# Kernel optimization log

Measured on AMD Instinct MI355X. Metric: run time of the kernel, lower is better.

## Reference

```python
import jax, jax.numpy as jnp
import numpy as np

EMBED_DIM = 768
NUM_HEAD = 12
HEAD_DIM = EMBED_DIM // NUM_HEAD


def setup_inputs() -> dict:
    key = jax.random.key(0)
    ks = jax.random.split(key, 9)
    B, S, E = 1, 4096, EMBED_DIM
    s = 1.0 / np.sqrt(E)
    inp = {
        "x": jax.random.normal(ks[0], (B, S, E), dtype=jnp.float32),
        "mask": jnp.zeros((B, S), dtype=jnp.bool_),  # True = masked out (padding)
        "Wq": jax.random.normal(ks[1], (E, E), dtype=jnp.float32) * s,
        "bq": jnp.zeros((E,), dtype=jnp.float32),
        "Wk": jax.random.normal(ks[2], (E, E), dtype=jnp.float32) * s,
        "bk": jnp.zeros((E,), dtype=jnp.float32),
        "Wv": jax.random.normal(ks[3], (E, E), dtype=jnp.float32) * s,
        "bv": jnp.zeros((E,), dtype=jnp.float32),
        "Wo": jax.random.normal(ks[4], (E, E), dtype=jnp.float32) * s,
        "bo": jnp.zeros((E,), dtype=jnp.float32),
    }
    return inp


def reference(x, mask, Wq, bq, Wk, bk, Wv, bv, Wo, bo):
    B, S, E = x.shape
    H, D = NUM_HEAD, HEAD_DIM
    # QKV projections -> [B, H, S, D]
    q = (x @ Wq.T + bq).reshape(B, S, H, D).transpose(0, 2, 1, 3)
    k = (x @ Wk.T + bk).reshape(B, S, H, D).transpose(0, 2, 1, 3)
    v = (x @ Wv.T + bv).reshape(B, S, H, D).transpose(0, 2, 1, 3)
    # NOTE: original scales by sqrt(embed_dim), not sqrt(head_dim)
    attn = jnp.einsum("bhqd,bhkd->bhqk", q, k) / jnp.sqrt(jnp.float32(E))
    # mask: [B, S] -> broadcast over (head, query) dims; True -> -inf
    attn = jnp.where(mask[:, None, None, :], -jnp.inf, attn)
    attn = jax.nn.softmax(attn, axis=-1)  # same math as manual max-subtract softmax
    out = jnp.einsum("bhqk,bhkd->bhqd", attn, v)  # [B, H, S, D]
    out = out.transpose(0, 2, 1, 3).reshape(B, S, E)
    return out @ Wo.T + bo
```

## Files before the change

### kernel.cpp

```cpp
#include <hip/hip_runtime.h>
#include <hip/hip_bf16.h>
#include <math.h>

typedef __bf16 bf16;
typedef __attribute__((ext_vector_type(8))) __bf16 bf16x8;
typedef __attribute__((ext_vector_type(4))) __bf16 bf16x4;
typedef __attribute__((ext_vector_type(4))) float f32x4;
typedef __attribute__((ext_vector_type(16))) float f32x16;

typedef __attribute__((address_space(1))) void* as1ptr;
typedef __attribute__((address_space(3))) void* as3ptr;

__device__ __forceinline__ void gload16(const void* g, void* lds) {
  __builtin_amdgcn_global_load_lds((as1ptr)(unsigned long long)(g),
                                   (as3ptr)(unsigned long long)(lds), 16, 0, 0);
}

#define MFMA16(a, b, c) __builtin_amdgcn_mfma_f32_16x16x32_bf16((a), (b), (c), 0, 0, 0)
#define MFMA32(a, b, c) __builtin_amdgcn_mfma_f32_32x32x16_bf16((a), (b), (c), 0, 0, 0)
#define EXP2(x) __builtin_amdgcn_exp2f(x)
#define WAITV4 asm volatile("s_waitcnt vmcnt(4)" ::: "memory")
#define WAITV2 asm volatile("s_waitcnt vmcnt(2)" ::: "memory")
#define WAITV0 asm volatile("s_waitcnt vmcnt(0)" ::: "memory")
#define BAR() __builtin_amdgcn_s_barrier()
#define PRIO1() __builtin_amdgcn_s_setprio(1)
#define PRIO0() __builtin_amdgcn_s_setprio(0)

#define SEQ 4096
#define EMB 768
#define QSC (0.036084391824351615f * 1.4426950408889634f)

#define NCVT 2688
__global__ __launch_bounds__(256)
void cvt_all_kernel(const float* __restrict__ x, const float* __restrict__ Wq,
                    const float* __restrict__ Wk, const float* __restrict__ Wv,
                    const float* __restrict__ Wo,
                    bf16* __restrict__ xb, bf16* __restrict__ Wqb, bf16* __restrict__ Wkb,
                    bf16* __restrict__ Wvb, bf16* __restrict__ Wob,
                    const unsigned char* __restrict__ mask,
                    unsigned long long* __restrict__ tf64) {
  int b = blockIdx.x;
  if (b == NCVT) {
    int t = threadIdx.x;
    if (t < 64) {
      unsigned v = 0;
      const unsigned char* mp = mask + t * 64;
      for (int i = 0; i < 64; i++) v |= mp[i];
      unsigned long long bits = __ballot(v != 0);
      if (t == 0) *tf64 = bits;
    }
    return;
  }
  const float* in;
  bf16* out;
  int base;
  if (b < 1536) {
    in = x; out = xb; base = b;
  } else {
    int r = b - 1536, seg = r / 288, off = r % 288;
    in  = (seg == 0) ? Wq  : (seg == 1) ? Wk  : (seg == 2) ? Wv  : Wo;
    out = (seg == 0) ? Wqb : (seg == 1) ? Wkb : (seg == 2) ? Wvb : Wob;
    base = off;
  }
  int i = (base * 256 + threadIdx.x) * 8;
  float4 a = *(const float4*)(in + i);
  float4 c = *(const float4*)(in + i + 4);
  bf16x8 v;
  v[0] = (bf16)a.x; v[1] = (bf16)a.y; v[2] = (bf16)a.z; v[3] = (bf16)a.w;
  v[4] = (bf16)c.x; v[5] = (bf16)c.y; v[6] = (bf16)c.z; v[7] = (bf16)c.w;
  *(bf16x8*)(out + i) = v;
}

template <int MODE>
__global__ __launch_bounds__(256)
void gemm_bt_kernel(const bf16* __restrict__ A,
                    const bf16* __restrict__ B0, const bf16* __restrict__ B1,
                    const bf16* __restrict__ B2,
                    const float* __restrict__ bias0, const float* __restrict__ bias1,
                    const float* __restrict__ bias2,
                    float* __restrict__ outF, bf16* __restrict__ Qh,
                    char* __restrict__ Kswz, char* __restrict__ Vswz) {
  __shared__ __attribute__((aligned(16))) char Asb[3][8192];
  __shared__ __attribute__((aligned(16))) char Bsb[3][8192];
  const int tid = threadIdx.x;
  const int wid = tid >> 6, lane = tid & 63;
  const int g = lane >> 4, c16 = lane & 15;
  const int wr = wid >> 1, wc = wid & 1;
  const int bm0 = blockIdx.x * 128;

  const bf16* Bp;
  const float* bias;
  int nb, mat = 0;
  if (MODE == 1) {
    mat = blockIdx.y / 6;
    nb = (blockIdx.y % 6) * 128;
    Bp = (mat == 0) ? B0 : (mat == 1 ? B1 : B2);
    bias = (mat == 0) ? bias0 : (mat == 1 ? bias1 : bias2);
  } else {
    nb = blockIdx.y * 128;
    Bp = B0;
    bias = bias0;
  }

  const int arow = tid >> 2, acol = (tid & 3) * 16;

#define STAGE_G(k, b)                                                              \
  do {                                                                             \
    gload16((const char*)A + (size_t)(bm0 + arow) * (EMB * 2) + (k)*64 + acol,     \
            &Asb[b][wid * 1024]);                                                  \
    gload16((const char*)A + (size_t)(bm0 + 64 + arow) * (EMB * 2) + (k)*64 + acol,\
            &Asb[b][4096 + wid * 1024]);                                           \
    gload16((const char*)Bp + (size_t)(nb + arow) * (EMB * 2) + (k)*64 + acol,     \
            &Bsb[b][wid * 1024]);                                                  \
    gload16((const char*)Bp + (size_t)(nb + 64 + arow) * (EMB * 2) + (k)*64 + acol,\
            &Bsb[b][4096 + wid * 1024]);                                           \
  } while (0)

  f32x4 acc[4][4];
#pragma unroll
  for (int i = 0; i < 4; i++)
#pragma unroll
    for (int j = 0; j < 4; j++) acc[i][j] = f32x4{0.f, 0.f, 0.f, 0.f};

#define COMPUTE_G(cur)                                                         \
  do {                                                                         \
    bf16x8 a[4], b[4];                                                         \
    _Pragma("unroll") for (int i = 0; i < 4; i++)                              \
        a[i] = *(const bf16x8*)(&Asb[cur][(wr * 64 + i * 16 + c16) * 64 + g * 16]); \
    _Pragma("unroll") for (int j = 0; j < 4; j++)                              \
        b[j] = *(const bf16x8*)(&Bsb[cur][(wc * 64 + j * 16 + c16) * 64 + g * 16]); \
    PRIO1();                                                                   \
    _Pragma("unroll") for (int i = 0; i < 4; i++)                              \
        _Pragma("unroll") for (int j = 0; j < 4; j++)                          \
            acc[i][j] = MFMA16(a[i], b[j], acc[i][j]);                         \
    PRIO0();                                                                   \
  } while (0)

  STAGE_G(0, 0);
  STAGE_G(1, 1);
  int cur = 0;
  for (int kk = 0; kk < EMB / 32 - 1; ++kk) {
    WAITV4;
    BAR();
    if (kk < EMB / 32 - 2) {
      int stb = (cur == 0) ? 2 : cur - 1;
      STAGE_G(kk + 2, stb);
    }
    COMPUTE_G(cur);
    cur = (cur == 2) ? 0 : cur + 1;
  }
  WAITV0;
  BAR();
  COMPUTE_G(cur);
#undef STAGE_G
#undef COMPUTE_G

#pragma unroll
  for (int i = 0; i < 4; i++) {
#pragma unroll
    for (int j = 0; j < 4; j++) {
      int colL = nb + wc * 64 + j * 16 + c16;
      float bval = bias[colL];
#pragma unroll
      for (int r = 0; r < 4; r++) {
        int row = bm0 + wr * 64 + i * 16 + 4 * g + r;
        float val = acc[i][j][r] + bval;
        if (MODE == 0) {
          outF[(size_t)row * EMB + colL] = val;
        } else {
          int hh = colL >> 6, d = colL & 63;
          if (mat == 0) {
            Qh[((size_t)hh * SEQ + row) * 64 + d] = (bf16)(val * QSC);
          } else if (mat == 1) {
            *(bf16*)(Kswz + ((size_t)hh * SEQ + row) * 128 +
                     ((d * 2) ^ ((row & 7) << 4))) = (bf16)val;
          } else {
            int kk2 = row & 63;
            int cc = (kk2 & 48) | (kk2 & 3) | ((kk2 & 4) << 1) | ((kk2 & 8) >> 1);
            *(bf16*)(Vswz + ((size_t)hh * 64 + d) * 8192 + (size_t)(row >> 6) * 128 +
                     ((cc * 2) ^ ((d & 7) << 4))) = (bf16)val;
          }
        }
      }
    }
  }
}

__global__ __launch_bounds__(512)
void attn_kernel(const char* __restrict__ Kswz, const char* __restrict__ Vswz,
                 const bf16* __restrict__ Qh, const unsigned char* __restrict__ mask,
                 const unsigned long long* __restrict__ tf64,
                 bf16* __restrict__ P0, bf16* __restrict__ P1, float* __restrict__ lm) {
  __shared__ __attribute__((aligned(16))) char LBUF[49152];
  char* LK = LBUF;
  char* LV = LBUF + 24576;
  const int tid = threadIdx.x;
  const int wid = tid >> 6, lane = tid & 63;
  const int qh = wid >> 1, kh = wid & 1;
  const int l31 = lane & 31, hi = lane >> 5;
  const int bsw = ((blockIdx.x & 7) * 96) + (blockIdx.x >> 3);
  const int h = bsw >> 6;
  const int rem = bsw & 63;
  const int qb = rem >> 1;
  const int ks = rem & 1;
  const unsigned long long tfb = *tf64;
  const int NT = 32;

  bf16x8 qa[4];
  {
    const bf16* qp = Qh + ((size_t)h * SEQ + qb * 128 + qh * 32 + l31) * 64 + hi * 8;
    qa[0] = *(const bf16x8*)(qp);
    qa[1] = *(const bf16x8*)(qp + 16);
    qa[2] = *(const bf16x8*)(qp + 32);
    qa[3] = *(const bf16x8*)(qp + 48);
  }

  f32x16 ot0, ot1;
#pragma unroll
  for (int r = 0; r < 16; r++) { ot0[r] = 0.f; ot1[r] = 0.f; }
  float l_ = 0.f;

  const char* ksrc = Kswz + (size_t)h * SEQ * 128 + (size_t)ks * 2048 * 128 + tid * 16;
  const char* vsrc = Vswz + ((size_t)h * 64 + (tid >> 3)) * 8192 + ks * 4096 + (tid & 7) * 16;

#define STAGE(t, b)                                              \
  do {                                                           \
    gload16(ksrc + (size_t)(t)*8192, LK + (b)*8192 + wid * 1024);\
    gload16(vsrc + (size_t)(t)*128,  LV + (b)*8192 + wid * 1024);\
  } while (0)

  const int krow = kh * 32 + l31;
  const int ksw = (krow & 7) << 4;
  const int vsw = (l31 & 7) << 4;
  const int vcb = kh * 64 + hi * 16;

#define COMPUTE(t, cur)                                                          \
  do {                                                                           \
    const char* Kb = LK + (cur)*8192;                                            \
    const char* Vb = LV + (cur)*8192;                                            \
    bf16x8 kf0 = *(const bf16x8*)(Kb + krow * 128 + ((hi * 16) ^ ksw));          \
    bf16x8 kf1 = *(const bf16x8*)(Kb + krow * 128 + ((32 + hi * 16) ^ ksw));     \
    bf16x8 kf2 = *(const bf16x8*)(Kb + krow * 128 + ((64 + hi * 16) ^ ksw));     \
    bf16x8 kf3 = *(const bf16x8*)(Kb + krow * 128 + ((96 + hi * 16) ^ ksw));     \
    f32x16 s;                                                                    \
    _Pragma("unroll") for (int r = 0; r < 16; r++) s[r] = 0.f;                   \
    PRIO1();                                                                     \
    s = MFMA32(kf0, qa[0], s);                                                   \
    s = MFMA32(kf1, qa[1], s);                                                   \
    s = MFMA32(kf2, qa[2], s);                                                   \
    s = MFMA32(kf3, qa[3], s);                                                   \
    PRIO0();                                                                     \
    if (tfb & (1ull << (ks * 32 + (t)))) {                                       \
      _Pragma("unroll") for (int r = 0; r < 16; r++) {                           \
        int key = ks * 2048 + (t)*64 + kh * 32 + (r & 3) + 8 * (r >> 2) + 4 * hi;\
        if (mask[key]) s[r] = -INFINITY;                                         \
      }                                                                          \
    }                                                                            \
    float p[16];                                                                 \
    _Pragma("unroll") for (int r = 0; r < 16; r++) p[r] = EXP2(s[r]);            \
    float ls = (((p[0] + p[1]) + (p[2] + p[3])) + ((p[4] + p[5]) + (p[6] + p[7]))) + \
               (((p[8] + p[9]) + (p[10] + p[11])) + ((p[12] + p[13]) + (p[14] + p[15]))); \
    l_ += ls;                                                                    \
    bf16x8 pb0, pb1;                                                             \
    _Pragma("unroll") for (int e = 0; e < 8; ++e) {                              \
      pb0[e] = (bf16)p[e];                                                       \
      pb1[e] = (bf16)p[8 + e];                                                   \
    }                                                                            \
    bf16x8 vf00 = *(const bf16x8*)(Vb + l31 * 128 + ((vcb) ^ vsw));              \
    bf16x8 vf01 = *(const bf16x8*)(Vb + l31 * 128 + ((vcb + 32) ^ vsw));         \
    bf16x8 vf10 = *(const bf16x8*)(Vb + (32 + l31) * 128 + ((vcb) ^ vsw));       \
    bf16x8 vf11 = *(const bf16x8*)(Vb + (32 + l31) * 128 + ((vcb + 32) ^ vsw));  \
    PRIO1();                                                                     \
    ot0 = MFMA32(vf00, pb0, ot0);                                                \
    ot0 = MFMA32(vf01, pb1, ot0);                                                \
    ot1 = MFMA32(vf10, pb0, ot1);                                                \
    ot1 = MFMA32(vf11, pb1, ot1);                                                \
    PRIO0();                                                                     \
  } while (0)

  STAGE(0, 0);
  STAGE(1, 1);
  int cur = 0;
  for (int t = 0; t < NT - 1; ++t) {
    WAITV2;
    BAR();
    if (t < NT - 2) {
      int stb = (cur == 0) ? 2 : cur - 1;
      STAGE(t + 2, stb);
    }
    COMPUTE(t, cur);
    cur = (cur == 2) ? 0 : cur + 1;
  }
  WAITV0;
  BAR();
  COMPUTE(NT - 1, cur);
#undef STAGE
#undef COMPUTE

  l_ += __shfl_xor(l_, 32);

  __syncthreads();
  float* ml = (float*)(LBUF + 32768);
  ml[wid * 64 + lane] = l_;
  __syncthreads();
  const int pw = wid ^ 1;
  float lt = l_ + ml[pw * 64 + lane];
  char* obase = LBUF + qh * 8192 + lane * 128;
  const int osw = (lane & 7) << 4;
  if (kh == 1) {
#pragma unroll
    for (int u = 0; u < 4; ++u) {
      *(f32x4*)(obase + ((u * 16) ^ osw)) =
          f32x4{ot0[4 * u], ot0[4 * u + 1], ot0[4 * u + 2], ot0[4 * u + 3]};
      *(f32x4*)(obase + (((4 + u) * 16) ^ osw)) =
          f32x4{ot1[4 * u], ot1[4 * u + 1], ot1[4 * u + 2], ot1[4 * u + 3]};
    }
  }
  __syncthreads();
  if (kh == 0) {
    float inv = 1.f / lt;
    int tok = qb * 128 + qh * 32 + l31;
    bf16* Op = ks ? P1 : P0;
    bf16* op = Op + (size_t)tok * EMB + h * 64;
#pragma unroll
    for (int u = 0; u < 4; ++u) {
      f32x4 w0 = *(const f32x4*)(obase + ((u * 16) ^ osw));
      f32x4 w1 = *(const f32x4*)(obase + (((4 + u) * 16) ^ osw));
      bf16x4 o0, o1;
#pragma unroll
      for (int e = 0; e < 4; ++e) {
        o0[e] = (bf16)((ot0[4 * u + e] + w0[e]) * inv);
        o1[e] = (bf16)((ot1[4 * u + e] + w1[e]) * inv);
      }
      *(bf16x4*)(op + 8 * u + 4 * hi) = o0;
      *(bf16x4*)(op + 32 + 8 * u + 4 * hi) = o1;
    }
    if (lane < 32) {
      lm[(((size_t)ks * 12 + h) * 4096 + tok) * 2 + 1] = lt;
    }
  }
}

__global__ __launch_bounds__(256)
void merge_kernel(bf16* __restrict__ P0, const bf16* __restrict__ P1,
                  const float* __restrict__ lm) {
  int idx = (blockIdx.x * 256 + threadIdx.x) * 8;
  int tok = idx / EMB;
  int e0 = idx % EMB;
  int h = e0 >> 6;
  float l0 = lm[((size_t)h * 4096 + tok) * 2 + 1];
  float l1 = lm[(((size_t)12 + h) * 4096 + tok) * 2 + 1];
  float inv = 1.f / (l0 + l1);
  float w0 = l0 * inv;
  float w1 = l1 * inv;
  bf16x8 a = *(const bf16x8*)(P0 + idx);
  bf16x8 b = *(const bf16x8*)(P1 + idx);
  bf16x8 o;
#pragma unroll
  for (int e = 0; e < 8; ++e) o[e] = (bf16)(w0 * (float)a[e] + w1 * (float)b[e]);
  *(bf16x8*)(P0 + idx) = o;
}

extern "C" void kernel_launch(void* const* d_in, const int* in_sizes, int n_in,
                              void* d_out, int out_size, void* d_ws, size_t ws_size,
                              hipStream_t stream) {
  (void)in_sizes; (void)n_in; (void)out_size; (void)ws_size;
  const float* x = (const float*)d_in[0];
  const unsigned char* mask = (const unsigned char*)d_in[1];
  const float* Wq = (const float*)d_in[2];
  const float* bq = (const float*)d_in[3];
  const float* Wk = (const float*)d_in[4];
  const float* bk = (const float*)d_in[5];
  const float* Wv = (const float*)d_in[6];
  const float* bv = (const float*)d_in[7];
  const float* Wo = (const float*)d_in[8];
  const float* bo = (const float*)d_in[9];
  float* out = (float*)d_out;
  char* ws = (char*)d_ws;

  bf16* xb   = (bf16*)(ws + 0);
  bf16* Wqb  = (bf16*)(ws + 6291456);
  bf16* Wkb  = (bf16*)(ws + 7471104);
  bf16* Wvb  = (bf16*)(ws + 8650752);
  bf16* Wob  = (bf16*)(ws + 9830400);
  bf16* Qh   = (bf16*)(ws + 11010048);
  char* Kswz = ws + 17301504;
  char* Vswz = ws + 23592960;
  bf16* Obuf = (bf16*)(ws + 29884416);
  unsigned long long* tf64 = (unsigned long long*)(ws + 36175872);
  float* lmArr = (float*)(ws + 36179968);
  bf16* P1 = xb;

  cvt_all_kernel<<<NCVT + 1, 256, 0, stream>>>(x, Wq, Wk, Wv, Wo, xb, Wqb, Wkb, Wvb,
                                               Wob, mask, tf64);
  gemm_bt_kernel<1><<<dim3(32, 18), 256, 0, stream>>>(
      xb, Wqb, Wkb, Wvb, bq, bk, bv, nullptr, Qh, Kswz, Vswz);
  attn_kernel<<<768, 512, 0, stream>>>(Kswz, Vswz, Qh, mask, tf64, Obuf, P1, lmArr);
  merge_kernel<<<1536, 256, 0, stream>>>(Obuf, P1, lmArr);
  gemm_bt_kernel<0><<<dim3(32, 6), 256, 0, stream>>>(
      Obuf, Wob, nullptr, nullptr, bo, nullptr, nullptr, out, nullptr, nullptr, nullptr);
}
```

Measured before the change: 124.2 us.

## Split attention keys four ways with 4-wave blocks each computing two query tiles

The attention kernel moves from 512-thread blocks with a 2-way key split to 256-thread blocks with a 4-way key split. Each wave now computes two 32-row query tiles against the same K/V fragments, so every LDS load feeds twice as many MFMAs. The staging pipeline drops from three buffers to two, with a full vmcnt wait each iteration. The merge kernel now combines four partials, two of them parked in the output buffer, which adds merge traffic and reduces how far loads run ahead of compute.

```diff
diff --git a/kernel.cpp b/kernel.cpp
--- a/kernel.cpp
+++ b/kernel.cpp
@@ -20,7 +20,6 @@
 #define MFMA32(a, b, c) __builtin_amdgcn_mfma_f32_32x32x16_bf16((a), (b), (c), 0, 0, 0)
 #define EXP2(x) __builtin_amdgcn_exp2f(x)
 #define WAITV4 asm volatile("s_waitcnt vmcnt(4)" ::: "memory")
-#define WAITV2 asm volatile("s_waitcnt vmcnt(2)" ::: "memory")
 #define WAITV0 asm volatile("s_waitcnt vmcnt(0)" ::: "memory")
 #define BAR() __builtin_amdgcn_s_barrier()
 #define PRIO1() __builtin_amdgcn_s_setprio(1)
@@ -186,48 +185,52 @@
   }
 }
 
-__global__ __launch_bounds__(512)
+__global__ __launch_bounds__(256)
 void attn_kernel(const char* __restrict__ Kswz, const char* __restrict__ Vswz,
                  const bf16* __restrict__ Qh, const unsigned char* __restrict__ mask,
                  const unsigned long long* __restrict__ tf64,
-                 bf16* __restrict__ P0, bf16* __restrict__ P1, float* __restrict__ lm) {
-  __shared__ __attribute__((aligned(16))) char LBUF[49152];
-  char* LK = LBUF;
-  char* LV = LBUF + 24576;
+                 bf16* __restrict__ P0, bf16* __restrict__ P1,
+                 bf16* __restrict__ P2, bf16* __restrict__ P3, float* __restrict__ lm) {
+  __shared__ __attribute__((aligned(16))) char LBUF[32768];
   const int tid = threadIdx.x;
   const int wid = tid >> 6, lane = tid & 63;
   const int qh = wid >> 1, kh = wid & 1;
   const int l31 = lane & 31, hi = lane >> 5;
-  const int bsw = ((blockIdx.x & 7) * 96) + (blockIdx.x >> 3);
-  const int h = bsw >> 6;
-  const int rem = bsw & 63;
-  const int qb = rem >> 1;
-  const int ks = rem & 1;
+  const int bsw = ((blockIdx.x & 7) * 192) + (blockIdx.x >> 3);
+  const int h = bsw >> 7;
+  const int rem = bsw & 127;
+  const int qb = rem >> 2;
+  const int ks = rem & 3;
   const unsigned long long tfb = *tf64;
-  const int NT = 32;
-
-  bf16x8 qa[4];
+  const int NT = 16;
+
+  const char* ksrc = Kswz + (size_t)h * SEQ * 128 + (size_t)ks * 1024 * 128 + tid * 16;
+  const char* vsrc = Vswz + ((size_t)h * 64 + (tid >> 3)) * 8192 + ks * 2048 + (tid & 7) * 16;
+
+#define STAGE(t, b)                                                             \
+  do {                                                                          \
+    gload16(ksrc + (size_t)(t)*8192,        LBUF + (b)*16384 + wid * 1024);     \
+    gload16(ksrc + (size_t)(t)*8192 + 4096, LBUF + (b)*16384 + 4096 + wid * 1024); \
+    gload16(vsrc + (size_t)(t)*128,             LBUF + (b)*16384 + 8192 + wid * 1024); \
+    gload16(vsrc + 32 * 8192 + (size_t)(t)*128, LBUF + (b)*16384 + 12288 + wid * 1024); \
+  } while (0)
+
+  STAGE(0, 0);
+
+  bf16x8 qaA[4], qaB[4];
   {
-    const bf16* qp = Qh + ((size_t)h * SEQ + qb * 128 + qh * 32 + l31) * 64 + hi * 8;
-    qa[0] = *(const bf16x8*)(qp);
-    qa[1] = *(const bf16x8*)(qp + 16);
-    qa[2] = *(const bf16x8*)(qp + 32);
-    qa[3] = *(const bf16x8*)(qp + 48);
-  }
-
-  f32x16 ot0, ot1;
-#pragma unroll
-  for (int r = 0; r < 16; r++) { ot0[r] = 0.f; ot1[r] = 0.f; }
-  float l_ = 0.f;
-
-  const char* ksrc = Kswz + (size_t)h * SEQ * 128 + (size_t)ks * 2048 * 128 + tid * 16;
-  const char* vsrc = Vswz + ((size_t)h * 64 + (tid >> 3)) * 8192 + ks * 4096 + (tid & 7) * 16;
-
-#define STAGE(t, b)                                              \
-  do {                                                           \
-    gload16(ksrc + (size_t)(t)*8192, LK + (b)*8192 + wid * 1024);\
-    gload16(vsrc + (size_t)(t)*128,  LV + (b)*8192 + wid * 1024);\
-  } while (0)
+    const bf16* qp = Qh + ((size_t)h * SEQ + qb * 128 + qh * 64 + l31) * 64 + hi * 8;
+#pragma unroll
+    for (int j = 0; j < 4; ++j) {
+      qaA[j] = *(const bf16x8*)(qp + j * 16);
+      qaB[j] = *(const bf16x8*)(qp + 32 * 64 + j * 16);
+    }
+  }
+
+  f32x16 otA0, otA1, otB0, otB1;
+#pragma unroll
+  for (int r = 0; r < 16; r++) { otA0[r] = 0.f; otA1[r] = 0.f; otB0[r] = 0.f; otB1[r] = 0.f; }
+  float lA_ = 0.f, lB_ = 0.f;
 
   const int krow = kh * 32 + l31;
   const int ksw = (krow & 7) << 4;
@@ -236,128 +239,170 @@
 
 #define COMPUTE(t, cur)                                                          \
   do {                                                                           \
-    const char* Kb = LK + (cur)*8192;                                            \
-    const char* Vb = LV + (cur)*8192;                                            \
+    const char* Kb = LBUF + (cur)*16384;                                         \
+    const char* Vb = Kb + 8192;                                                  \
     bf16x8 kf0 = *(const bf16x8*)(Kb + krow * 128 + ((hi * 16) ^ ksw));          \
     bf16x8 kf1 = *(const bf16x8*)(Kb + krow * 128 + ((32 + hi * 16) ^ ksw));     \
     bf16x8 kf2 = *(const bf16x8*)(Kb + krow * 128 + ((64 + hi * 16) ^ ksw));     \
     bf16x8 kf3 = *(const bf16x8*)(Kb + krow * 128 + ((96 + hi * 16) ^ ksw));     \
-    f32x16 s;                                                                    \
-    _Pragma("unroll") for (int r = 0; r < 16; r++) s[r] = 0.f;                   \
+    f32x16 sA, sB;                                                               \
+    _Pragma("unroll") for (int r = 0; r < 16; r++) { sA[r] = 0.f; sB[r] = 0.f; } \
     PRIO1();                                                                     \
-    s = MFMA32(kf0, qa[0], s);                                                   \
-    s = MFMA32(kf1, qa[1], s);                                                   \
-    s = MFMA32(kf2, qa[2], s);                                                   \
-    s = MFMA32(kf3, qa[3], s);                                                   \
+    sA = MFMA32(kf0, qaA[0], sA);                                                \
+    sB = MFMA32(kf0, qaB[0], sB);                                                \
+    sA = MFMA32(kf1, qaA[1], sA);                                                \
+    sB = MFMA32(kf1, qaB[1], sB);                                                \
+    sA = MFMA32(kf2, qaA[2], sA);                                                \
+    sB = MFMA32(kf2, qaB[2], sB);                                                \
+    sA = MFMA32(kf3, qaA[3], sA);                                                \
+    sB = MFMA32(kf3, qaB[3], sB);                                                \
     PRIO0();                                                                     \
-    if (tfb & (1ull << (ks * 32 + (t)))) {                                       \
+    if (tfb & (1ull << (ks * 16 + (t)))) {                                       \
       _Pragma("unroll") for (int r = 0; r < 16; r++) {                           \
-        int key = ks * 2048 + (t)*64 + kh * 32 + (r & 3) + 8 * (r >> 2) + 4 * hi;\
-        if (mask[key]) s[r] = -INFINITY;                                         \
+        int key = ks * 1024 + (t)*64 + kh * 32 + (r & 3) + 8 * (r >> 2) + 4 * hi;\
+        if (mask[key]) { sA[r] = -INFINITY; sB[r] = -INFINITY; }                 \
       }                                                                          \
     }                                                                            \
-    float p[16];                                                                 \
-    _Pragma("unroll") for (int r = 0; r < 16; r++) p[r] = EXP2(s[r]);            \
-    float ls = (((p[0] + p[1]) + (p[2] + p[3])) + ((p[4] + p[5]) + (p[6] + p[7]))) + \
-               (((p[8] + p[9]) + (p[10] + p[11])) + ((p[12] + p[13]) + (p[14] + p[15]))); \
-    l_ += ls;                                                                    \
-    bf16x8 pb0, pb1;                                                             \
-    _Pragma("unroll") for (int e = 0; e < 8; ++e) {                              \
-      pb0[e] = (bf16)p[e];                                                       \
-      pb1[e] = (bf16)p[8 + e];                                                   \
+    bf16x8 pbA0, pbA1, pbB0, pbB1;                                               \
+    {                                                                            \
+      _Pragma("unroll") for (int r = 0; r < 16; r++) sA[r] = EXP2(sA[r]);        \
+      lA_ += (((sA[0] + sA[1]) + (sA[2] + sA[3])) + ((sA[4] + sA[5]) + (sA[6] + sA[7]))) + \
+             (((sA[8] + sA[9]) + (sA[10] + sA[11])) + ((sA[12] + sA[13]) + (sA[14] + sA[15]))); \
+      _Pragma("unroll") for (int e = 0; e < 8; ++e) {                            \
+        pbA0[e] = (bf16)sA[e];                                                   \
+        pbA1[e] = (bf16)sA[8 + e];                                               \
+      }                                                                          \
+    }                                                                            \
+    {                                                                            \
+      _Pragma("unroll") for (int r = 0; r < 16; r++) sB[r] = EXP2(sB[r]);        \
+      lB_ += (((sB[0] + sB[1]) + (sB[2] + sB[3])) + ((sB[4] + sB[5]) + (sB[6] + sB[7]))) + \
+             (((sB[8] + sB[9]) + (sB[10] + sB[11])) + ((sB[12] + sB[13]) + (sB[14] + sB[15]))); \
+      _Pragma("unroll") for (int e = 0; e < 8; ++e) {                            \
+        pbB0[e] = (bf16)sB[e];                                                   \
+        pbB1[e] = (bf16)sB[8 + e];                                               \
+      }                                                                          \
     }                                                                            \
     bf16x8 vf00 = *(const bf16x8*)(Vb + l31 * 128 + ((vcb) ^ vsw));              \
     bf16x8 vf01 = *(const bf16x8*)(Vb + l31 * 128 + ((vcb + 32) ^ vsw));         \
     bf16x8 vf10 = *(const bf16x8*)(Vb + (32 + l31) * 128 + ((vcb) ^ vsw));       \
     bf16x8 vf11 = *(const bf16x8*)(Vb + (32 + l31) * 128 + ((vcb + 32) ^ vsw));  \
     PRIO1();                                                                     \
-    ot0 = MFMA32(vf00, pb0, ot0);                                                \
-    ot0 = MFMA32(vf01, pb1, ot0);                                                \
-    ot1 = MFMA32(vf10, pb0, ot1);                                                \
-    ot1 = MFMA32(vf11, pb1, ot1);                                                \
+    otA0 = MFMA32(vf00, pbA0, otA0);                                             \
+    otB0 = MFMA32(vf00, pbB0, otB0);                                             \
+    otA0 = MFMA32(vf01, pbA1, otA0);                                             \
+    otB0 = MFMA32(vf01, pbB1, otB0);                                             \
+    otA1 = MFMA32(vf10, pbA0, otA1);                                             \
+    otB1 = MFMA32(vf10, pbB0, otB1);                                             \
+    otA1 = MFMA32(vf11, pbA1, otA1);                                             \
+    otB1 = MFMA32(vf11, pbB1, otB1);                                             \
     PRIO0();                                                                     \
   } while (0)
 
-  STAGE(0, 0);
-  STAGE(1, 1);
-  int cur = 0;
-  for (int t = 0; t < NT - 1; ++t) {
-    WAITV2;
+  for (int t = 0; t < NT; ++t) {
+    WAITV0;
     BAR();
-    if (t < NT - 2) {
-      int stb = (cur == 0) ? 2 : cur - 1;
-      STAGE(t + 2, stb);
-    }
-    COMPUTE(t, cur);
-    cur = (cur == 2) ? 0 : cur + 1;
-  }
-  WAITV0;
-  BAR();
-  COMPUTE(NT - 1, cur);
+    if (t < NT - 1) STAGE(t + 1, (t + 1) & 1);
+    COMPUTE(t, t & 1);
+  }
 #undef STAGE
 #undef COMPUTE
 
-  l_ += __shfl_xor(l_, 32);
+  lA_ += __shfl_xor(lA_, 32);
+  lB_ += __shfl_xor(lB_, 32);
 
   __syncthreads();
-  float* ml = (float*)(LBUF + 32768);
-  ml[wid * 64 + lane] = l_;
+  float* ml = (float*)(LBUF + 16384);
+  ml[(wid * 64 + lane) * 2 + 0] = lA_;
+  ml[(wid * 64 + lane) * 2 + 1] = lB_;
   __syncthreads();
   const int pw = wid ^ 1;
-  float lt = l_ + ml[pw * 64 + lane];
-  char* obase = LBUF + qh * 8192 + lane * 128;
+  const float ltA = lA_ + ml[(pw * 64 + lane) * 2 + 0];
+  const float ltB = lB_ + ml[(pw * 64 + lane) * 2 + 1];
+  bf16* Op = (ks == 0) ? P0 : (ks == 1) ? P1 : (ks == 2) ? P2 : P3;
+  char* pbase = LBUF + qh * 8192 + lane * 128;
   const int osw = (lane & 7) << 4;
+  const int tokA = qb * 128 + qh * 64 + l31;
   if (kh == 1) {
 #pragma unroll
     for (int u = 0; u < 4; ++u) {
-      *(f32x4*)(obase + ((u * 16) ^ osw)) =
-          f32x4{ot0[4 * u], ot0[4 * u + 1], ot0[4 * u + 2], ot0[4 * u + 3]};
-      *(f32x4*)(obase + (((4 + u) * 16) ^ osw)) =
-          f32x4{ot1[4 * u], ot1[4 * u + 1], ot1[4 * u + 2], ot1[4 * u + 3]};
+      *(f32x4*)(pbase + ((u * 16) ^ osw)) =
+          f32x4{otA0[4 * u], otA0[4 * u + 1], otA0[4 * u + 2], otA0[4 * u + 3]};
+      *(f32x4*)(pbase + (((4 + u) * 16) ^ osw)) =
+          f32x4{otA1[4 * u], otA1[4 * u + 1], otA1[4 * u + 2], otA1[4 * u + 3]};
     }
   }
   __syncthreads();
   if (kh == 0) {
-    float inv = 1.f / lt;
-    int tok = qb * 128 + qh * 32 + l31;
-    bf16* Op = ks ? P1 : P0;
-    bf16* op = Op + (size_t)tok * EMB + h * 64;
+    float inv = 1.f / ltA;
+    bf16* op = Op + (size_t)tokA * EMB + h * 64;
 #pragma unroll
     for (int u = 0; u < 4; ++u) {
-      f32x4 w0 = *(const f32x4*)(obase + ((u * 16) ^ osw));
-      f32x4 w1 = *(const f32x4*)(obase + (((4 + u) * 16) ^ osw));
+      f32x4 w0 = *(const f32x4*)(pbase + ((u * 16) ^ osw));
+      f32x4 w1 = *(const f32x4*)(pbase + (((4 + u) * 16) ^ osw));
       bf16x4 o0, o1;
 #pragma unroll
       for (int e = 0; e < 4; ++e) {
-        o0[e] = (bf16)((ot0[4 * u + e] + w0[e]) * inv);
-        o1[e] = (bf16)((ot1[4 * u + e] + w1[e]) * inv);
+        o0[e] = (bf16)((otA0[4 * u + e] + w0[e]) * inv);
+        o1[e] = (bf16)((otA1[4 * u + e] + w1[e]) * inv);
       }
       *(bf16x4*)(op + 8 * u + 4 * hi) = o0;
       *(bf16x4*)(op + 32 + 8 * u + 4 * hi) = o1;
     }
-    if (lane < 32) {
-      lm[(((size_t)ks * 12 + h) * 4096 + tok) * 2 + 1] = lt;
-    }
+    if (lane < 32) lm[(((size_t)ks * 12 + h) << 12) + tokA] = ltA;
+  }
+  __syncthreads();
+  if (kh == 1) {
+#pragma unroll
+    for (int u = 0; u < 4; ++u) {
+      *(f32x4*)(pbase + ((u * 16) ^ osw)) =
+          f32x4{otB0[4 * u], otB0[4 * u + 1], otB0[4 * u + 2], otB0[4 * u + 3]};
+      *(f32x4*)(pbase + (((4 + u) * 16) ^ osw)) =
+          f32x4{otB1[4 * u], otB1[4 * u + 1], otB1[4 * u + 2], otB1[4 * u + 3]};
+    }
+  }
+  __syncthreads();
+  if (kh == 0) {
+    float inv = 1.f / ltB;
+    bf16* op = Op + (size_t)(tokA + 32) * EMB + h * 64;
+#pragma unroll
+    for (int u = 0; u < 4; ++u) {
+      f32x4 w0 = *(const f32x4*)(pbase + ((u * 16) ^ osw));
+      f32x4 w1 = *(const f32x4*)(pbase + (((4 + u) * 16) ^ osw));
+      bf16x4 o0, o1;
+#pragma unroll
+      for (int e = 0; e < 4; ++e) {
+        o0[e] = (bf16)((otB0[4 * u + e] + w0[e]) * inv);
+        o1[e] = (bf16)((otB1[4 * u + e] + w1[e]) * inv);
+      }
+      *(bf16x4*)(op + 8 * u + 4 * hi) = o0;
+      *(bf16x4*)(op + 32 + 8 * u + 4 * hi) = o1;
+    }
+    if (lane < 32) lm[(((size_t)ks * 12 + h) << 12) + tokA + 32] = ltB;
   }
 }
 
 __global__ __launch_bounds__(256)
 void merge_kernel(bf16* __restrict__ P0, const bf16* __restrict__ P1,
+                  const bf16* __restrict__ P2, const bf16* __restrict__ P3,
                   const float* __restrict__ lm) {
   int idx = (blockIdx.x * 256 + threadIdx.x) * 8;
   int tok = idx / EMB;
-  int e0 = idx % EMB;
-  int h = e0 >> 6;
-  float l0 = lm[((size_t)h * 4096 + tok) * 2 + 1];
-  float l1 = lm[(((size_t)12 + h) * 4096 + tok) * 2 + 1];
-  float inv = 1.f / (l0 + l1);
-  float w0 = l0 * inv;
-  float w1 = l1 * inv;
+  int h = (idx % EMB) >> 6;
+  float l0 = lm[(((size_t)0 * 12 + h) << 12) + tok];
+  float l1 = lm[(((size_t)1 * 12 + h) << 12) + tok];
+  float l2 = lm[(((size_t)2 * 12 + h) << 12) + tok];
+  float l3 = lm[(((size_t)3 * 12 + h) << 12) + tok];
+  float inv = 1.f / ((l0 + l1) + (l2 + l3));
+  float w0 = l0 * inv, w1 = l1 * inv, w2 = l2 * inv, w3 = l3 * inv;
   bf16x8 a = *(const bf16x8*)(P0 + idx);
   bf16x8 b = *(const bf16x8*)(P1 + idx);
+  bf16x8 c = *(const bf16x8*)(P2 + idx);
+  bf16x8 d = *(const bf16x8*)(P3 + idx);
   bf16x8 o;
 #pragma unroll
-  for (int e = 0; e < 8; ++e) o[e] = (bf16)(w0 * (float)a[e] + w1 * (float)b[e]);
+  for (int e = 0; e < 8; ++e)
+    o[e] = (bf16)((w0 * (float)a[e] + w1 * (float)b[e]) +
+                  (w2 * (float)c[e] + w3 * (float)d[e]));
   *(bf16x8*)(P0 + idx) = o;
 }
 
@@ -390,13 +435,16 @@
   unsigned long long* tf64 = (unsigned long long*)(ws + 36175872);
   float* lmArr = (float*)(ws + 36179968);
   bf16* P1 = xb;
+  bf16* P2 = (bf16*)out;
+  bf16* P3 = (bf16*)out + (size_t)SEQ * EMB;
 
   cvt_all_kernel<<<NCVT + 1, 256, 0, stream>>>(x, Wq, Wk, Wv, Wo, xb, Wqb, Wkb, Wvb,
                                                Wob, mask, tf64);
   gemm_bt_kernel<1><<<dim3(32, 18), 256, 0, stream>>>(
       xb, Wqb, Wkb, Wvb, bq, bk, bv, nullptr, Qh, Kswz, Vswz);
-  attn_kernel<<<768, 512, 0, stream>>>(Kswz, Vswz, Qh, mask, tf64, Obuf, P1, lmArr);
-  merge_kernel<<<1536, 256, 0, stream>>>(Obuf, P1, lmArr);
+  attn_kernel<<<1536, 256, 0, stream>>>(Kswz, Vswz, Qh, mask, tf64, Obuf, P1, P2, P3,
+                                        lmArr);
+  merge_kernel<<<1536, 256, 0, stream>>>(Obuf, P1, P2, P3, lmArr);
   gemm_bt_kernel<0><<<dim3(32, 6), 256, 0, stream>>>(
       Obuf, Wob, nullptr, nullptr, bo, nullptr, nullptr, out, nullptr, nullptr, nullptr);
 }
```

Measured after the change: 136.3 us. +9.7%, slower.

## Split output GEMM into smaller-tile kernel and compute softmax row sums via MFMA

Applied to the files above, without the earlier changes.

The output projection now has its own kernel with 64x64 tiles, launching 768 blocks instead of 192 so the GPU's compute units are better occupied for this small GEMM. In attention, the per-lane scalar adds that built the softmax denominator are replaced by two extra MFMAs against an all-ones operand, which yield the row sums directly and also remove the cross-lane shuffle. This takes VALU work off the exp-heavy inner loop, but adds matrix-core work and an extra 16-register accumulator. The smaller GEMM tiles also reuse each loaded tile less.

```diff
diff --git a/kernel.cpp b/kernel.cpp
--- a/kernel.cpp
+++ b/kernel.cpp
@@ -71,15 +71,14 @@
   *(bf16x8*)(out + i) = v;
 }
 
-template <int MODE>
 __global__ __launch_bounds__(256)
-void gemm_bt_kernel(const bf16* __restrict__ A,
-                    const bf16* __restrict__ B0, const bf16* __restrict__ B1,
-                    const bf16* __restrict__ B2,
-                    const float* __restrict__ bias0, const float* __restrict__ bias1,
-                    const float* __restrict__ bias2,
-                    float* __restrict__ outF, bf16* __restrict__ Qh,
-                    char* __restrict__ Kswz, char* __restrict__ Vswz) {
+void gemm_qkv_kernel(const bf16* __restrict__ A,
+                     const bf16* __restrict__ B0, const bf16* __restrict__ B1,
+                     const bf16* __restrict__ B2,
+                     const float* __restrict__ bias0, const float* __restrict__ bias1,
+                     const float* __restrict__ bias2,
+                     bf16* __restrict__ Qh, char* __restrict__ Kswz,
+                     char* __restrict__ Vswz) {
   __shared__ __attribute__((aligned(16))) char Asb[3][8192];
   __shared__ __attribute__((aligned(16))) char Bsb[3][8192];
   const int tid = threadIdx.x;
@@ -88,19 +87,10 @@
   const int wr = wid >> 1, wc = wid & 1;
   const int bm0 = blockIdx.x * 128;
 
-  const bf16* Bp;
-  const float* bias;
-  int nb, mat = 0;
-  if (MODE == 1) {
-    mat = blockIdx.y / 6;
-    nb = (blockIdx.y % 6) * 128;
-    Bp = (mat == 0) ? B0 : (mat == 1 ? B1 : B2);
-    bias = (mat == 0) ? bias0 : (mat == 1 ? bias1 : bias2);
-  } else {
-    nb = blockIdx.y * 128;
-    Bp = B0;
-    bias = bias0;
-  }
+  const int mat = blockIdx.y / 6;
+  const int nb = (blockIdx.y % 6) * 128;
+  const bf16* Bp = (mat == 0) ? B0 : (mat == 1 ? B1 : B2);
+  const float* bias = (mat == 0) ? bias0 : (mat == 1 ? bias1 : bias2);
 
   const int arow = tid >> 2, acol = (tid & 3) * 16;
 
@@ -165,22 +155,92 @@
       for (int r = 0; r < 4; r++) {
         int row = bm0 + wr * 64 + i * 16 + 4 * g + r;
         float val = acc[i][j][r] + bval;
-        if (MODE == 0) {
-          outF[(size_t)row * EMB + colL] = val;
+        int hh = colL >> 6, d = colL & 63;
+        if (mat == 0) {
+          Qh[((size_t)hh * SEQ + row) * 64 + d] = (bf16)(val * QSC);
+        } else if (mat == 1) {
+          *(bf16*)(Kswz + ((size_t)hh * SEQ + row) * 128 +
+                   ((d * 2) ^ ((row & 7) << 4))) = (bf16)val;
         } else {
-          int hh = colL >> 6, d = colL & 63;
-          if (mat == 0) {
-            Qh[((size_t)hh * SEQ + row) * 64 + d] = (bf16)(val * QSC);
-          } else if (mat == 1) {
-            *(bf16*)(Kswz + ((size_t)hh * SEQ + row) * 128 +
-                     ((d * 2) ^ ((row & 7) << 4))) = (bf16)val;
-          } else {
-            int kk2 = row & 63;
-            int cc = (kk2 & 48) | (kk2 & 3) | ((kk2 & 4) << 1) | ((kk2 & 8) >> 1);
-            *(bf16*)(Vswz + ((size_t)hh * 64 + d) * 8192 + (size_t)(row >> 6) * 128 +
-                     ((cc * 2) ^ ((d & 7) << 4))) = (bf16)val;
-          }
+          int kk2 = row & 63;
+          int cc = (kk2 & 48) | (kk2 & 3) | ((kk2 & 4) << 1) | ((kk2 & 8) >> 1);
+          *(bf16*)(Vswz + ((size_t)hh * 64 + d) * 8192 + (size_t)(row >> 6) * 128 +
+                   ((cc * 2) ^ ((d & 7) << 4))) = (bf16)val;
         }
+      }
+    }
+  }
+}
+
+__global__ __launch_bounds__(256)
+void gemm_out_kernel(const bf16* __restrict__ A, const bf16* __restrict__ B,
+                     const float* __restrict__ bias, float* __restrict__ outF) {
+  __shared__ __attribute__((aligned(16))) char Asb[3][4096];
+  __shared__ __attribute__((aligned(16))) char Bsb[3][4096];
+  const int tid = threadIdx.x;
+  const int wid = tid >> 6, lane = tid & 63;
+  const int g = lane >> 4, c16 = lane & 15;
+  const int wr = wid >> 1, wc = wid & 1;
+  const int bm0 = blockIdx.x * 64, nb = blockIdx.y * 64;
+  const int arow = tid >> 2, acol = (tid & 3) * 16;
+
+#define STAGE_O(k, b)                                                          \
+  do {                                                                         \
+    gload16((const char*)A + (size_t)(bm0 + arow) * (EMB * 2) + (k)*64 + acol, \
+            &Asb[b][wid * 1024]);                                              \
+    gload16((const char*)B + (size_t)(nb + arow) * (EMB * 2) + (k)*64 + acol,  \
+            &Bsb[b][wid * 1024]);                                              \
+  } while (0)
+
+  f32x4 acc[2][2];
+#pragma unroll
+  for (int i = 0; i < 2; i++)
+#pragma unroll
+    for (int j = 0; j < 2; j++) acc[i][j] = f32x4{0.f, 0.f, 0.f, 0.f};
+
+#define COMPUTE_O(cur)                                                         \
+  do {                                                                         \
+    bf16x8 a[2], b[2];                                                         \
+    _Pragma("unroll") for (int i = 0; i < 2; i++)                              \
+        a[i] = *(const bf16x8*)(&Asb[cur][(wr * 32 + i * 16 + c16) * 64 + g * 16]); \
+    _Pragma("unroll") for (int j = 0; j < 2; j++)                              \
+        b[j] = *(const bf16x8*)(&Bsb[cur][(wc * 32 + j * 16 + c16) * 64 + g * 16]); \
+    PRIO1();                                                                   \
+    _Pragma("unroll") for (int i = 0; i < 2; i++)                              \
+        _Pragma("unroll") for (int j = 0; j < 2; j++)                          \
+            acc[i][j] = MFMA16(a[i], b[j], acc[i][j]);                         \
+    PRIO0();                                                                   \
+  } while (0)
+
+  STAGE_O(0, 0);
+  STAGE_O(1, 1);
+  int cur = 0;
+  for (int kk = 0; kk < EMB / 32 - 1; ++kk) {
+    WAITV2;
+    BAR();
+    if (kk < EMB / 32 - 2) {
+      int stb = (cur == 0) ? 2 : cur - 1;
+      STAGE_O(kk + 2, stb);
+    }
+    COMPUTE_O(cur);
+    cur = (cur == 2) ? 0 : cur + 1;
+  }
+  WAITV0;
+  BAR();
+  COMPUTE_O(cur);
+#undef STAGE_O
+#undef COMPUTE_O
+
+#pragma unroll
+  for (int i = 0; i < 2; i++) {
+#pragma unroll
+    for (int j = 0; j < 2; j++) {
+      int colL = nb + wc * 32 + j * 16 + c16;
+      float bval = bias[colL];
+#pragma unroll
+      for (int r = 0; r < 4; r++) {
+        int row = bm0 + wr * 32 + i * 16 + 4 * g + r;
+        outF[(size_t)row * EMB + colL] = acc[i][j][r] + bval;
       }
     }
   }
@@ -214,11 +274,13 @@
     qa[2] = *(const bf16x8*)(qp + 32);
     qa[3] = *(const bf16x8*)(qp + 48);
   }
-
-  f32x16 ot0, ot1;
-#pragma unroll
-  for (int r = 0; r < 16; r++) { ot0[r] = 0.f; ot1[r] = 0.f; }
-  float l_ = 0.f;
+  bf16x8 onesA;
+#pragma unroll
+  for (int e = 0; e < 8; ++e) onesA[e] = (bf16)1.0f;
+
+  f32x16 ot0, ot1, lacc;
+#pragma unroll
+  for (int r = 0; r < 16; r++) { ot0[r] = 0.f; ot1[r] = 0.f; lacc[r] = 0.f; }
 
   const char* ksrc = Kswz + (size_t)h * SEQ * 128 + (size_t)ks * 2048 * 128 + tid * 16;
   const char* vsrc = Vswz + ((size_t)h * 64 + (tid >> 3)) * 8192 + ks * 4096 + (tid & 7) * 16;
@@ -258,9 +320,6 @@
     }                                                                            \
     float p[16];                                                                 \
     _Pragma("unroll") for (int r = 0; r < 16; r++) p[r] = EXP2(s[r]);            \
-    float ls = (((p[0] + p[1]) + (p[2] + p[3])) + ((p[4] + p[5]) + (p[6] + p[7]))) + \
-               (((p[8] + p[9]) + (p[10] + p[11])) + ((p[12] + p[13]) + (p[14] + p[15]))); \
-    l_ += ls;                                                                    \
     bf16x8 pb0, pb1;                                                             \
     _Pragma("unroll") for (int e = 0; e < 8; ++e) {                              \
       pb0[e] = (bf16)p[e];                                                       \
@@ -275,6 +334,8 @@
     ot0 = MFMA32(vf01, pb1, ot0);                                                \
     ot1 = MFMA32(vf10, pb0, ot1);                                                \
     ot1 = MFMA32(vf11, pb1, ot1);                                                \
+    lacc = MFMA32(onesA, pb0, lacc);                                             \
+    lacc = MFMA32(onesA, pb1, lacc);                                             \
     PRIO0();                                                                     \
   } while (0)
 
@@ -297,7 +358,7 @@
 #undef STAGE
 #undef COMPUTE
 
-  l_ += __shfl_xor(l_, 32);
+  float l_ = lacc[0];
 
   __syncthreads();
   float* ml = (float*)(LBUF + 32768);
@@ -393,10 +454,9 @@
 
   cvt_all_kernel<<<NCVT + 1, 256, 0, stream>>>(x, Wq, Wk, Wv, Wo, xb, Wqb, Wkb, Wvb,
                                                Wob, mask, tf64);
-  gemm_bt_kernel<1><<<dim3(32, 18), 256, 0, stream>>>(
-      xb, Wqb, Wkb, Wvb, bq, bk, bv, nullptr, Qh, Kswz, Vswz);
+  gemm_qkv_kernel<<<dim3(32, 18), 256, 0, stream>>>(
+      xb, Wqb, Wkb, Wvb, bq, bk, bv, Qh, Kswz, Vswz);
   attn_kernel<<<768, 512, 0, stream>>>(Kswz, Vswz, Qh, mask, tf64, Obuf, P1, lmArr);
   merge_kernel<<<1536, 256, 0, stream>>>(Obuf, P1, lmArr);
-  gemm_bt_kernel<0><<<dim3(32, 6), 256, 0, stream>>>(
-      Obuf, Wob, nullptr, nullptr, bo, nullptr, nullptr, out, nullptr, nullptr, nullptr);
-}
+  gemm_out_kernel<<<dim3(64, 12), 256, 0, stream>>>(Obuf, Wob, bo, out);
+}
```

Result: no change. 123.2 us (median of 2 runs) (-0.8%).
